# Performance work log

Hardware: AMD Instinct MI355X
Metric: run time of the kernel (lower is better)

## Reference

```python
import jax, jax.numpy as jnp
import numpy as np

N = 100000
E = 1600000
D = 128
EPS = 1e-12  # torch F.normalize default eps


def _sage_conv(x, src, dst, Wl, bl, Wr):
    # mean-aggregate neighbor features: for each dst node, mean of x[src]
    msg = x[src]                                              # [E, D] gather
    s = jax.ops.segment_sum(msg, dst, num_segments=x.shape[0])
    cnt = jax.ops.segment_sum(jnp.ones((dst.shape[0],), x.dtype), dst,
                              num_segments=x.shape[0])
    agg = s / jnp.maximum(cnt, 1.0)[:, None]                  # isolated nodes -> 0
    out = agg @ Wl + bl + x @ Wr                              # lin_l(aggr) + lin_r(x)
    nrm = jnp.linalg.norm(out, axis=-1, keepdims=True)        # L2 normalize
    return out / jnp.maximum(nrm, EPS)


def setup_inputs() -> dict:
    key = jax.random.key(0)
    ks = jax.random.split(key, 8)
    x = jax.random.normal(ks[0], (N, D), dtype=jnp.float32)
    edge_index = jax.random.randint(ks[1], (2, E), 0, N, dtype=jnp.int64)
    sc = 1.0 / np.sqrt(D)
    Wl1 = jax.random.uniform(ks[2], (D, D), jnp.float32, -sc, sc)
    bl1 = jax.random.uniform(ks[3], (D,), jnp.float32, -sc, sc)
    Wr1 = jax.random.uniform(ks[4], (D, D), jnp.float32, -sc, sc)
    Wl2 = jax.random.uniform(ks[5], (D, D), jnp.float32, -sc, sc)
    bl2 = jax.random.uniform(ks[6], (D,), jnp.float32, -sc, sc)
    Wr2 = jax.random.uniform(ks[7], (D, D), jnp.float32, -sc, sc)
    return {"x": x, "edge_index": edge_index, "Wl1": Wl1, "bl1": bl1,
            "Wr1": Wr1, "Wl2": Wl2, "bl2": bl2, "Wr2": Wr2}


def reference(x, edge_index, Wl1, bl1, Wr1, Wl2, bl2, Wr2):
    src, dst = edge_index[0], edge_index[1]
    h = jax.nn.relu(_sage_conv(x, src, dst, Wl1, bl1, Wr1))
    # prev_h is None -> zeros, so residual add is identity
    h = jax.nn.relu(_sage_conv(h, src, dst, Wl2, bl2, Wr2))
    return h
```

## Files before the change

kernel.cpp:

```cpp
#include <hip/hip_runtime.h>

#define DD 128
#define NBMAX 2048
#define EPB 16384

typedef short bf16x8 __attribute__((ext_vector_type(8)));
typedef float f32x4  __attribute__((ext_vector_type(4)));

static __device__ __forceinline__ unsigned short f2b(float f) {
    union { float f; unsigned u; } v; v.f = f;
    unsigned u = v.u;
    return (unsigned short)((u + 0x7FFFu + ((u >> 16) & 1u)) >> 16);
}
static __device__ __forceinline__ float blo(unsigned p) {
    union { unsigned u; float f; } v; v.u = p << 16; return v.f;
}
static __device__ __forceinline__ float bhi(unsigned p) {
    union { unsigned u; float f; } v; v.u = p & 0xFFFF0000u; return v.f;
}

__global__ __launch_bounds__(256) void cvt_kernel(
    const float* __restrict__ X, unsigned short* __restrict__ Xb, int n8)
{
    int i = blockIdx.x * 256 + threadIdx.x;
    if (i >= n8) return;
    const float4* p = (const float4*)(X + (size_t)i * 8);
    float4 a = p[0], b = p[1];
    uint4 o;
    o.x = f2b(a.x) | ((unsigned)f2b(a.y) << 16);
    o.y = f2b(a.z) | ((unsigned)f2b(a.w) << 16);
    o.z = f2b(b.x) | ((unsigned)f2b(b.y) << 16);
    o.w = f2b(b.z) | ((unsigned)f2b(b.w) << 16);
    *(uint4*)(Xb + (size_t)i * 8) = o;
}

__global__ __launch_bounds__(1024) void bhist_kernel(
    const int* __restrict__ dst, int* __restrict__ bcnt, int nE, int nbuck)
{
    __shared__ int hist[NBMAX];
    const int tid = threadIdx.x;
    const int e0 = blockIdx.x * EPB;
    const int e1 = min(e0 + EPB, nE);

    for (int b = tid; b < nbuck; b += 1024) hist[b] = 0;
    __syncthreads();
    for (int e = e0 + tid; e < e1; e += 1024)
        atomicAdd(&hist[dst[e] >> 6], 1);
    __syncthreads();
    for (int b = tid; b < nbuck; b += 1024) {
        int c = hist[b];
        if (c) atomicAdd(&bcnt[b], c);
    }
}

__global__ __launch_bounds__(1024) void bscan_kernel(
    const int* __restrict__ bcnt, int* __restrict__ bbase,
    int* __restrict__ gcur, int* __restrict__ rowptr, int nbuck, int n, int nE)
{
    __shared__ int tmp[1024];
    __shared__ int carry;
    int t = threadIdx.x;
    if (t == 0) carry = 0;
    __syncthreads();
    for (int c0 = 0; c0 < nbuck; c0 += 1024) {
        int v = (c0 + t < nbuck) ? bcnt[c0 + t] : 0;
        tmp[t] = v;
        __syncthreads();
        for (int off = 1; off < 1024; off <<= 1) {
            int u = (t >= off) ? tmp[t - off] : 0;
            __syncthreads();
            tmp[t] += u;
            __syncthreads();
        }
        int excl = carry + tmp[t] - v;
        if (c0 + t < nbuck) { bbase[c0 + t] = excl; gcur[c0 + t] = excl; }
        __syncthreads();
        if (t == 1023) carry += tmp[1023];
        __syncthreads();
    }
    if (t == 0) { bbase[nbuck] = nE; rowptr[n] = nE; }
}

__global__ __launch_bounds__(1024) void coarse_kernel(
    const int* __restrict__ src, const int* __restrict__ dst,
    int* __restrict__ gcur, int* __restrict__ pairs, int nE, int nbuck)
{
    __shared__ int hist[NBMAX];
    const int tid = threadIdx.x;
    const int e0 = blockIdx.x * EPB;
    const int e1 = min(e0 + EPB, nE);

    for (int b = tid; b < nbuck; b += 1024) hist[b] = 0;
    __syncthreads();
    for (int e = e0 + tid; e < e1; e += 1024)
        atomicAdd(&hist[dst[e] >> 6], 1);
    __syncthreads();
    for (int b = tid; b < nbuck; b += 1024) {
        int c = hist[b];
        hist[b] = c ? atomicAdd(&gcur[b], c) : 0;
    }
    __syncthreads();
    for (int e = e0 + tid; e < e1; e += 1024) {
        int d = dst[e];
        int p = atomicAdd(&hist[d >> 6], 1);
        pairs[p] = src[e] | ((d & 63) << 17);
    }
}

__global__ __launch_bounds__(256) void fine_kernel(
    const int* __restrict__ pairs, const int* __restrict__ bbase,
    int* __restrict__ rowptr, int* __restrict__ csr, int n)
{
    __shared__ int cnt[64];
    __shared__ int excl[64];
    __shared__ int cur[64];
    const int tid   = threadIdx.x;
    const int node0 = blockIdx.x * 64;
    const int nn    = min(64, n - node0);
    const int base  = bbase[blockIdx.x];
    const int wend  = bbase[blockIdx.x + 1];

    if (tid < 64) cnt[tid] = 0;
    __syncthreads();
    for (int j = base + tid; j < wend; j += 256)
        atomicAdd(&cnt[pairs[j] >> 17], 1);
    __syncthreads();
    if (tid == 0) {
        int run = 0;
        #pragma unroll
        for (int i = 0; i < 64; ++i) { excl[i] = run; run += cnt[i]; }
    }
    __syncthreads();
    if (tid < nn) {
        int rp = base + excl[tid];
        rowptr[node0 + tid] = rp;
        cur[tid] = rp;
    }
    __syncthreads();
    for (int j = base + tid; j < wend; j += 256) {
        int e = pairs[j];
        int p = atomicAdd(&cur[e >> 17], 1);
        csr[p] = e & 131071;
    }
}

__global__ __launch_bounds__(256) void deg_kernel(
    const int* __restrict__ dst, int* __restrict__ deg, int nE)
{
    int e = blockIdx.x * 256 + threadIdx.x;
    if (e < nE) atomicAdd(&deg[dst[e]], 1);
}

__global__ __launch_bounds__(256) void scan1_kernel(
    const int* __restrict__ deg, int* __restrict__ inc,
    int* __restrict__ bsum, int n)
{
    __shared__ int tmp[256];
    int i = blockIdx.x * 256 + threadIdx.x;
    int t = threadIdx.x;
    tmp[t] = (i < n) ? deg[i] : 0;
    __syncthreads();
    for (int off = 1; off < 256; off <<= 1) {
        int v = (t >= off) ? tmp[t - off] : 0;
        __syncthreads();
        tmp[t] += v;
        __syncthreads();
    }
    if (i < n) inc[i] = tmp[t];
    if (t == 255) bsum[blockIdx.x] = tmp[255];
}

__global__ __launch_bounds__(512) void scan2_kernel(int* __restrict__ bsum, int nb)
{
    __shared__ int tmp[512];
    int t = threadIdx.x;
    tmp[t] = (t < nb) ? bsum[t] : 0;
    __syncthreads();
    for (int off = 1; off < 512; off <<= 1) {
        int v = (t >= off) ? tmp[t - off] : 0;
        __syncthreads();
        tmp[t] += v;
        __syncthreads();
    }
    if (t < nb) bsum[t] = (t == 0) ? 0 : tmp[t - 1];
}

__global__ __launch_bounds__(256) void scan3_kernel(
    const int* __restrict__ inc, const int* __restrict__ bsum,
    int* __restrict__ rowptr, int* __restrict__ cursor, int n)
{
    int i = blockIdx.x * 256 + threadIdx.x;
    if (i > n) return;
    int rp = (i == 0) ? 0 : (inc[i - 1] + bsum[(i - 1) >> 8]);
    rowptr[i] = rp;
    if (i < n) cursor[i] = rp;
}

__global__ __launch_bounds__(256) void fill_kernel(
    const int* __restrict__ src, const int* __restrict__ dst,
    int* __restrict__ cursor, int* __restrict__ csr, int nE)
{
    int e = blockIdx.x * 256 + threadIdx.x;
    if (e < nE) {
        int pos = atomicAdd(&cursor[dst[e]], 1);
        csr[pos] = src[e];
    }
}

__global__ __launch_bounds__(256) void wprep_kernel(
    const float* __restrict__ Wl, const float* __restrict__ Wr,
    unsigned short* __restrict__ Wp)
{
    int t = blockIdx.x * 256 + threadIdx.x;
    if (t >= 4096) return;
    int l  = t & 63;
    int nt = (t >> 6) & 7;
    int kk = t >> 9;
    int c  = nt * 16 + (l & 15);
    int k0 = kk * 32 + (l >> 4) * 8;
    unsigned short o[8];
    #pragma unroll
    for (int j = 0; j < 8; ++j) {
        int k = k0 + j;
        float v = (k < 128) ? Wl[k * 128 + c] : Wr[(k - 128) * 128 + c];
        o[j] = f2b(v);
    }
    uint4 pk;
    pk.x = o[0] | ((unsigned)o[1] << 16);
    pk.y = o[2] | ((unsigned)o[3] << 16);
    pk.z = o[4] | ((unsigned)o[5] << 16);
    pk.w = o[6] | ((unsigned)o[7] << 16);
    *(uint4*)(Wp + (size_t)t * 8) = pk;
}

static __device__ __forceinline__ void acc8(float* a, uint4 v) {
    a[0] += blo(v.x); a[1] += bhi(v.x);
    a[2] += blo(v.y); a[3] += bhi(v.y);
    a[4] += blo(v.z); a[5] += bhi(v.z);
    a[6] += blo(v.w); a[7] += bhi(v.w);
}

__global__ __launch_bounds__(256, 4) void fused_kernel(
    const unsigned short* __restrict__ Xb,
    const int* __restrict__ csr,
    const int* __restrict__ rowptr,
    const unsigned short* __restrict__ Wp,
    const float* __restrict__ bl,
    float* __restrict__ Y,
    unsigned short* __restrict__ Hb,
    int n, int writeY, int writeH)
{
    __shared__ unsigned short Slds[64 * DD];

    const int tid  = threadIdx.x;
    const int row0 = blockIdx.x * 64;
    const int l    = tid & 15;
    const int grp  = tid >> 4;
    const int gb   = tid & 48;
    const unsigned short* __restrict__ xsl = Xb + l * 8;

    for (int round = 0; round < 4; ++round) {
        const int nl   = grp + 16 * round;
        const int node = row0 + nl;
        if (node < n) {
            const int beg = rowptr[node];
            const int deg = rowptr[node + 1] - beg;
            uint4 o;
            if (deg == 0) {
                o = make_uint4(0u, 0u, 0u, 0u);
            } else {
                float a[8]  = {0.f,0.f,0.f,0.f,0.f,0.f,0.f,0.f};
                float b8[8] = {0.f,0.f,0.f,0.f,0.f,0.f,0.f,0.f};
                uint4 va[8], vb[8];
                int cv = csr[beg + min(l, deg - 1)];

#define AGG_ISSUE(buf, jj)                                          \
    {                                                               \
        const int qb = (jj) & 8;                                    \
        _Pragma("unroll")                                           \
        for (int q = 0; q < 8; ++q) {                               \
            int s = __shfl(cv, gb | (qb + q));                      \
            buf[q] = *(const uint4*)(xsl + (size_t)s * DD);         \
        }                                                           \
    }
                AGG_ISSUE(va, 0);
                int j = 0;
                for (;;) {
                    if (j + 8 >= deg) {
                        int cnt = deg - j;
                        #pragma unroll
                        for (int q = 0; q < 8; ++q)
                            if (q < cnt) acc8((q & 1) ? b8 : a, va[q]);
                        break;
                    }
                    {
                        int jj = j + 8;
                        if ((jj & 15) == 0) cv = csr[beg + min(jj + l, deg - 1)];
                        AGG_ISSUE(vb, jj);
                    }
                    #pragma unroll
                    for (int q = 0; q < 8; ++q) acc8((q & 1) ? b8 : a, va[q]);
                    j += 8;
                    if (j + 8 >= deg) {
                        int cnt = deg - j;
                        #pragma unroll
                        for (int q = 0; q < 8; ++q)
                            if (q < cnt) acc8((q & 1) ? b8 : a, vb[q]);
                        break;
                    }
                    {
                        int jj = j + 8;
                        if ((jj & 15) == 0) cv = csr[beg + min(jj + l, deg - 1)];
                        AGG_ISSUE(va, jj);
                    }
                    #pragma unroll
                    for (int q = 0; q < 8; ++q) acc8((q & 1) ? b8 : a, vb[q]);
                    j += 8;
                }
#undef AGG_ISSUE
                const float iv = 1.0f / (float)deg;
                float r[8];
                #pragma unroll
                for (int i = 0; i < 8; ++i) r[i] = (a[i] + b8[i]) * iv;
                o.x = f2b(r[0]) | ((unsigned)f2b(r[1]) << 16);
                o.y = f2b(r[2]) | ((unsigned)f2b(r[3]) << 16);
                o.z = f2b(r[4]) | ((unsigned)f2b(r[5]) << 16);
                o.w = f2b(r[6]) | ((unsigned)f2b(r[7]) << 16);
            }
            *(uint4*)(Slds + nl * DD + ((l ^ (nl & 15)) << 3)) = o;
        }
    }
    __syncthreads();

    const int wid = tid >> 6;
    const int l64 = tid & 63;
    const int lr  = l64 & 15;
    const int lk  = l64 >> 4;
    const int r   = wid * 16 + lr;

    int arow = row0 + r;
    if (arow >= n) arow = n - 1;
    const size_t abase = (size_t)arow * DD + lk * 8;

    f32x4 acc[8];
    #pragma unroll
    for (int t = 0; t < 8; ++t) acc[t] = (f32x4){0.f, 0.f, 0.f, 0.f};

    const bf16x8* wp = (const bf16x8*)Wp + l64;

    #pragma unroll
    for (int kk = 0; kk < 8; ++kk) {
        bf16x8 afrag;
        if (kk < 4) {
            const int c = kk * 4 + lk;
            afrag = *(const bf16x8*)(Slds + r * DD + (((c ^ lr)) << 3));
        } else {
            afrag = *(const bf16x8*)(Xb + abase + (kk - 4) * 32);
        }
        #pragma unroll
        for (int t = 0; t < 8; ++t) {
            bf16x8 bfrag = wp[(kk * 8 + t) * 64];
            acc[t] = __builtin_amdgcn_mfma_f32_16x16x32_bf16(afrag, bfrag, acc[t], 0, 0, 0);
        }
    }

    float bv[8];
    #pragma unroll
    for (int t = 0; t < 8; ++t) bv[t] = bl[t * 16 + lr];

    #pragma unroll
    for (int j = 0; j < 4; ++j) {
        float ss = 0.f;
        #pragma unroll
        for (int t = 0; t < 8; ++t) {
            acc[t][j] += bv[t];
            ss += acc[t][j] * acc[t][j];
        }
        ss += __shfl_xor(ss, 1);
        ss += __shfl_xor(ss, 2);
        ss += __shfl_xor(ss, 4);
        ss += __shfl_xor(ss, 8);
        float sc = 1.0f / fmaxf(sqrtf(ss), 1e-12f);

        int g = row0 + wid * 16 + lk * 4 + j;
        if (g < n) {
            #pragma unroll
            for (int t = 0; t < 8; ++t) {
                float o = fmaxf(acc[t][j] * sc, 0.f);
                if (writeY) Y[(size_t)g * DD + t * 16 + lr] = o;
                if (writeH) Hb[(size_t)g * DD + t * 16 + lr] = f2b(o);
            }
        }
    }
}

extern "C" void kernel_launch(void* const* d_in, const int* in_sizes, int n_in,
                              void* d_out, int out_size, void* d_ws, size_t ws_size,
                              hipStream_t stream)
{
    const float* x   = (const float*)d_in[0];
    const int*   ei  = (const int*)d_in[1];
    const float* Wl1 = (const float*)d_in[2];
    const float* bl1 = (const float*)d_in[3];
    const float* Wr1 = (const float*)d_in[4];
    const float* Wl2 = (const float*)d_in[5];
    const float* bl2 = (const float*)d_in[6];
    const float* Wr2 = (const float*)d_in[7];
    float* out = (float*)d_out;

    const int N = in_sizes[0] / DD;
    const int E = in_sizes[1] / 2;
    const int* src = ei;
    const int* dst = ei + E;

    char* w = (char*)d_ws;
    size_t off = 0;
    auto alloc = [&](size_t bytes) {
        void* p = w + off;
        off += (bytes + 255) & ~(size_t)255;
        return p;
    };
    unsigned short* xb  = (unsigned short*)alloc((size_t)N * DD * 2);
    unsigned short* hb  = (unsigned short*)alloc((size_t)N * DD * 2);
    int*   csr    = (int*)  alloc((size_t)E * sizeof(int));
    int*   deg    = (int*)  alloc((size_t)N * sizeof(int));
    int*   inc    = (int*)  alloc((size_t)N * sizeof(int));
    int*   rowptr = (int*)  alloc((size_t)(N + 1) * sizeof(int));
    int*   cursor = (int*)  alloc((size_t)N * sizeof(int));
    int*   bsum   = (int*)  alloc(512 * sizeof(int));
    unsigned short* Wp1 = (unsigned short*)alloc(4096 * 8 * 2);
    unsigned short* Wp2 = (unsigned short*)alloc(4096 * 8 * 2);
    int*   gcur   = (int*)  alloc(NBMAX * sizeof(int));
    int*   bcnt   = (int*)  alloc(NBMAX * sizeof(int));
    int*   bbase  = (int*)  alloc((NBMAX + 1) * sizeof(int));
    int*   pairs  = (int*)hb;
    (void)ws_size;

    const int nbuck = (N + 63) / 64;
    const int nebl  = (E + EPB - 1) / EPB;

    cvt_kernel<<<(N * DD / 8 + 255) / 256, 256, 0, stream>>>(x, xb, N * DD / 8);

    if (N <= 131072 && nbuck <= NBMAX) {
        hipMemsetAsync(bcnt, 0, (size_t)nbuck * sizeof(int), stream);
        bhist_kernel <<<nebl, 1024, 0, stream>>>(dst, bcnt, E, nbuck);
        bscan_kernel <<<1, 1024, 0, stream>>>(bcnt, bbase, gcur, rowptr, nbuck, N, E);
        coarse_kernel<<<nebl, 1024, 0, stream>>>(src, dst, gcur, pairs, E, nbuck);
        fine_kernel  <<<nbuck, 256, 0, stream>>>(pairs, bbase, rowptr, csr, N);
    } else {
        const int nb = (N + 255) / 256;
        hipMemsetAsync(deg, 0, (size_t)N * sizeof(int), stream);
        deg_kernel  <<<(E + 255) / 256, 256, 0, stream>>>(dst, deg, E);
        scan1_kernel<<<nb, 256, 0, stream>>>(deg, inc, bsum, N);
        scan2_kernel<<<1, 512, 0, stream>>>(bsum, nb);
        scan3_kernel<<<(N + 256) / 256, 256, 0, stream>>>(inc, bsum, rowptr, cursor, N);
        fill_kernel <<<(E + 255) / 256, 256, 0, stream>>>(src, dst, cursor, csr, E);
    }
    wprep_kernel<<<16, 256, 0, stream>>>(Wl1, Wr1, Wp1);
    wprep_kernel<<<16, 256, 0, stream>>>(Wl2, Wr2, Wp2);

    const int grid = (N + 63) / 64;

    fused_kernel<<<grid, 256, 0, stream>>>(xb, csr, rowptr, Wp1, bl1,
                                           out, hb, N, 0, 1);
    fused_kernel<<<grid, 256, 0, stream>>>(hb, csr, rowptr, Wp2, bl2,
                                           out, nullptr, N, 1, 0);
}
```

Baseline: 218.5 us.

## Halve fused block size, prefetch CSR indices early, merge weight-prep launches

Measured after the change: 509.8 us. 2.33x slower.

```diff
diff --git a/kernel.cpp b/kernel.cpp
--- a/kernel.cpp
+++ b/kernel.cpp
@@ -207,15 +207,22 @@
     }
 }
 
-__global__ __launch_bounds__(256) void wprep_kernel(
-    const float* __restrict__ Wl, const float* __restrict__ Wr,
-    unsigned short* __restrict__ Wp)
+__global__ __launch_bounds__(256) void wprep2_kernel(
+    const float* __restrict__ Wl1, const float* __restrict__ Wr1,
+    const float* __restrict__ Wl2, const float* __restrict__ Wr2,
+    unsigned short* __restrict__ Wp1, unsigned short* __restrict__ Wp2)
 {
     int t = blockIdx.x * 256 + threadIdx.x;
-    if (t >= 4096) return;
-    int l  = t & 63;
-    int nt = (t >> 6) & 7;
-    int kk = t >> 9;
+    if (t >= 8192) return;
+    const int which = t >> 12;
+    const int tt = t & 4095;
+    const float* __restrict__ Wl = which ? Wl2 : Wl1;
+    const float* __restrict__ Wr = which ? Wr2 : Wr1;
+    unsigned short* __restrict__ Wp = which ? Wp2 : Wp1;
+
+    int l  = tt & 63;
+    int nt = (tt >> 6) & 7;
+    int kk = tt >> 9;
     int c  = nt * 16 + (l & 15);
     int k0 = kk * 32 + (l >> 4) * 8;
     unsigned short o[8];
@@ -230,7 +237,7 @@
     pk.y = o[2] | ((unsigned)o[3] << 16);
     pk.z = o[4] | ((unsigned)o[5] << 16);
     pk.w = o[6] | ((unsigned)o[7] << 16);
-    *(uint4*)(Wp + (size_t)t * 8) = pk;
+    *(uint4*)(Wp + (size_t)tt * 8) = pk;
 }
 
 static __device__ __forceinline__ void acc8(float* a, uint4 v) {
@@ -240,7 +247,7 @@
     a[6] += blo(v.w); a[7] += bhi(v.w);
 }
 
-__global__ __launch_bounds__(256, 4) void fused_kernel(
+__global__ __launch_bounds__(128, 6) void fused_kernel(
     const unsigned short* __restrict__ Xb,
     const int* __restrict__ csr,
     const int* __restrict__ rowptr,
@@ -250,17 +257,17 @@
     unsigned short* __restrict__ Hb,
     int n, int writeY, int writeH)
 {
-    __shared__ unsigned short Slds[64 * DD];
+    __shared__ unsigned short Slds[32 * DD];
 
     const int tid  = threadIdx.x;
-    const int row0 = blockIdx.x * 64;
+    const int row0 = blockIdx.x * 32;
     const int l    = tid & 15;
     const int grp  = tid >> 4;
     const int gb   = tid & 48;
     const unsigned short* __restrict__ xsl = Xb + l * 8;
 
     for (int round = 0; round < 4; ++round) {
-        const int nl   = grp + 16 * round;
+        const int nl   = grp + 8 * round;
         const int node = row0 + nl;
         if (node < n) {
             const int beg = rowptr[node];
@@ -273,6 +280,7 @@
                 float b8[8] = {0.f,0.f,0.f,0.f,0.f,0.f,0.f,0.f};
                 uint4 va[8], vb[8];
                 int cv = csr[beg + min(l, deg - 1)];
+                int cvn;
 
 #define AGG_ISSUE(buf, jj)                                          \
     {                                                               \
@@ -282,6 +290,12 @@
             int s = __shfl(cv, gb | (qb + q));                      \
             buf[q] = *(const uint4*)(xsl + (size_t)s * DD);         \
         }                                                           \
+    }
+#define CV_STEP(jj)                                                 \
+    {                                                               \
+        if (((jj) & 15) == 0) cv = cvn;                             \
+        else if ((jj) + 8 < deg)                                    \
+            cvn = csr[beg + min((jj) + 8 + l, deg - 1)];            \
     }
                 AGG_ISSUE(va, 0);
                 int j = 0;
@@ -295,7 +309,7 @@
                     }
                     {
                         int jj = j + 8;
-                        if ((jj & 15) == 0) cv = csr[beg + min(jj + l, deg - 1)];
+                        CV_STEP(jj);
                         AGG_ISSUE(vb, jj);
                     }
                     #pragma unroll
@@ -310,7 +324,7 @@
                     }
                     {
                         int jj = j + 8;
-                        if ((jj & 15) == 0) cv = csr[beg + min(jj + l, deg - 1)];
+                        CV_STEP(jj);
                         AGG_ISSUE(va, jj);
                     }
                     #pragma unroll
@@ -318,6 +332,7 @@
                     j += 8;
                 }
 #undef AGG_ISSUE
+#undef CV_STEP
                 const float iv = 1.0f / (float)deg;
                 float r[8];
                 #pragma unroll
@@ -353,7 +368,7 @@
         bf16x8 afrag;
         if (kk < 4) {
             const int c = kk * 4 + lk;
-            afrag = *(const bf16x8*)(Slds + r * DD + (((c ^ lr)) << 3));
+            afrag = *(const bf16x8*)(Slds + r * DD + ((c ^ lr) << 3));
         } else {
             afrag = *(const bf16x8*)(Xb + abase + (kk - 4) * 32);
         }
@@ -456,13 +471,12 @@
         scan3_kernel<<<(N + 256) / 256, 256, 0, stream>>>(inc, bsum, rowptr, cursor, N);
         fill_kernel <<<(E + 255) / 256, 256, 0, stream>>>(src, dst, cursor, csr, E);
     }
-    wprep_kernel<<<16, 256, 0, stream>>>(Wl1, Wr1, Wp1);
-    wprep_kernel<<<16, 256, 0, stream>>>(Wl2, Wr2, Wp2);
-
-    const int grid = (N + 63) / 64;
-
-    fused_kernel<<<grid, 256, 0, stream>>>(xb, csr, rowptr, Wp1, bl1,
+    wprep2_kernel<<<32, 256, 0, stream>>>(Wl1, Wr1, Wl2, Wr2, Wp1, Wp2);
+
+    const int grid = (N + 31) / 32;
+
+    fused_kernel<<<grid, 128, 0, stream>>>(xb, csr, rowptr, Wp1, bl1,
                                            out, hb, N, 0, 1);
-    fused_kernel<<<grid, 256, 0, stream>>>(hb, csr, rowptr, Wp2, bl2,
+    fused_kernel<<<grid, 128, 0, stream>>>(hb, csr, rowptr, Wp2, bl2,
                                            out, nullptr, N, 1, 0);
 }
```
